# Kernel optimization log

Measured on AMD Instinct MI355X. Metric: run time of the kernel, lower is better.

Reference implementation:

```python
import jax, jax.numpy as jnp
import numpy as np

B, S, SK = 4, 1024, 1024
Q_IN, KV_IN = 1024, 1024
G, DQ, DV = 16, 64, 64
OUT = Q_IN
EPS = 1e-5


def setup_inputs() -> dict:
    key = jax.random.key(0)
    ks = jax.random.split(key, 12)
    s_q = 1.0 / np.sqrt(Q_IN)
    s_kv = 1.0 / np.sqrt(KV_IN)
    s_p = 1.0 / np.sqrt(G * DV)
    return {
        "Q": jax.random.normal(ks[0], (B, S, Q_IN), jnp.float32),
        "KV": jax.random.normal(ks[1], (B, SK, KV_IN), jnp.float32),
        "Wq": jax.random.normal(ks[2], (G * DQ, Q_IN), jnp.float32) * s_q,
        "bq": jax.random.normal(ks[3], (G * DQ,), jnp.float32) * s_q,
        "Wk": jax.random.normal(ks[4], (G * DQ, KV_IN), jnp.float32) * s_kv,
        "bk": jax.random.normal(ks[5], (G * DQ,), jnp.float32) * s_kv,
        "Wv": jax.random.normal(ks[6], (G * DV, KV_IN), jnp.float32) * s_kv,
        "bv": jax.random.normal(ks[7], (G * DV,), jnp.float32) * s_kv,
        "Wp": jax.random.normal(ks[8], (OUT, G * DV), jnp.float32) * s_p,
        "bp": jax.random.normal(ks[9], (OUT,), jnp.float32) * s_p,
        "gamma": jnp.ones((OUT,), jnp.float32),
        "beta": jnp.zeros((OUT,), jnp.float32),
    }


def reference(Q, KV, Wq, bq, Wk, bk, Wv, bv, Wp, bp, gamma, beta):
    b, s, _ = Q.shape
    sk = KV.shape[1]
    inv_sqrt_dim = DQ ** (-0.5)

    # projections
    q = Q @ Wq.T + bq            # [b, s, G*DQ]
    k = KV @ Wk.T + bk           # [b, sk, G*DQ]
    v = KV @ Wv.T + bv           # [b, sk, G*DV]

    # q/k: group is the SLOW axis; v: group is the FAST axis (faithful to source)
    q = q.reshape(b, s, G, DQ)               # [b, s, g, d]
    k = k.reshape(b, sk, G, DQ)              # [b, sk, g, d]
    v = v.reshape(b, sk, DV, G)              # [b, sk, d, g]

    logits = jnp.einsum('bsgd,btgd->bgst', q, k) * inv_sqrt_dim  # [b, g, s, sk]
    scores = jax.nn.softmax(logits, axis=-1)
    attn = jnp.einsum('bgst,btdg->bgsd', scores, v)              # [b, g, s, dv]

    # flatten as (dv, g): feature index = d*G + g  (faithful to source permute)
    attn = attn.transpose(0, 2, 3, 1).reshape(b, s, DV * G)
    out = attn @ Wp.T + bp + Q

    # LayerNorm
    mu = out.mean(axis=-1, keepdims=True)
    var = out.var(axis=-1, keepdims=True)
    out = (out - mu) * jax.lax.rsqrt(var + EPS) * gamma + beta

    return out, scores.reshape(b * G, s, sk)
```

## Files before the change

kernel.cpp:

```cpp
#include <hip/hip_runtime.h>

typedef __attribute__((ext_vector_type(8))) short short8;
typedef __attribute__((ext_vector_type(4))) short s16x4;
typedef __attribute__((ext_vector_type(4))) float f32x4;

static __device__ __forceinline__ short f2bf(float x) {
  union { float f; unsigned u; } v; v.f = x;
  unsigned r = (v.u + 0x7fffu + ((v.u >> 16) & 1u)) >> 16;
  return (short)r;
}
static __device__ __forceinline__ float bf2f(short x) {
  union { unsigned u; float f; } v; v.u = ((unsigned)(unsigned short)x) << 16;
  return v.f;
}

static __device__ __forceinline__ void gld16(const short* g, short* l) {
  __builtin_amdgcn_global_load_lds(
      (const __attribute__((address_space(1))) unsigned*)g,
      (__attribute__((address_space(3))) unsigned*)l, 16, 0, 0);
}

static __device__ __forceinline__ void conv8(const float* __restrict__ src,
                                             short* __restrict__ dst, int i,
                                             float scale) {
  const f32x4* s = (const f32x4*)(src + (long)i * 8);
  f32x4 a = s[0], b = s[1];
  short8 o;
  o[0] = f2bf(a[0] * scale); o[1] = f2bf(a[1] * scale);
  o[2] = f2bf(a[2] * scale); o[3] = f2bf(a[3] * scale);
  o[4] = f2bf(b[0] * scale); o[5] = f2bf(b[1] * scale);
  o[6] = f2bf(b[2] * scale); o[7] = f2bf(b[3] * scale);
  *(short8*)(dst + (long)i * 8) = o;
}

__global__ __launch_bounds__(256) void prep(
    const float* __restrict__ Q, const float* __restrict__ KV,
    const float* __restrict__ Wq, const float* __restrict__ Wk,
    const float* __restrict__ Wv, const float* __restrict__ Wp,
    const float* __restrict__ bq,
    short* __restrict__ Qb, short* __restrict__ KVb,
    short* __restrict__ Wqb, short* __restrict__ Wkb,
    short* __restrict__ Wvb, short* __restrict__ Wpb,
    float* __restrict__ bqs) {
  const int blk = blockIdx.x, tid = threadIdx.x;
  if (blk < 2048) {
    conv8(Q, Qb, blk * 256 + tid, 1.f);
  } else if (blk < 4096) {
    conv8(KV, KVb, (blk - 2048) * 256 + tid, 1.f);
  } else if (blk < 4608) {
    conv8(Wq, Wqb, (blk - 4096) * 256 + tid, 0.125f);
  } else if (blk < 5120) {
    conv8(Wk, Wkb, (blk - 4608) * 256 + tid, 1.f);
  } else if (blk < 5632) {
    conv8(Wv, Wvb, (blk - 5120) * 256 + tid, 1.f);
  } else if (blk < 6656) {
    __shared__ float row[1024];
    const long o = blk - 5632;
    *(f32x4*)&row[tid * 4] = *(const f32x4*)(Wp + o * 1024 + tid * 4);
    __syncthreads();
    const int f0 = tid * 4;
    s16x4 t;
#pragma unroll
    for (int j = 0; j < 4; ++j) {
      int f = f0 + j;
      t[j] = f2bf(row[((f & 63) << 4) + (f >> 6)]);
    }
    *(s16x4*)(Wpb + o * 1024 + f0) = t;
  } else {
    int i = (blk - 6656) * 256 + tid;
    bqs[i] = bq[i] * 0.125f;
  }
}

template <typename OutT>
static __device__ __forceinline__ void gemm_core(
    const short* __restrict__ A, const short* __restrict__ B,
    OutT* __restrict__ C, const float* __restrict__ bias,
    const float* __restrict__ resid, int bm, int bn, int omode,
    short (*As)[128 * 64], short (*Bs)[128 * 64]) {
  const int tid = threadIdx.x, lane = tid & 63, wave = tid >> 6;
  const int fr = lane & 15, khi = lane >> 4;
  const int wr = wave >> 1, wc = wave & 1;

  f32x4 acc[4][4];
#pragma unroll
  for (int m = 0; m < 4; ++m)
#pragma unroll
    for (int n = 0; n < 4; ++n) acc[m][n] = (f32x4){0.f, 0.f, 0.f, 0.f};

  auto stage = [&](int buf, int k0) {
#pragma unroll
    for (int it = 0; it < 4; ++it) {
      int l = it * 256 + tid;
      int r = l >> 3, c = (l & 7) ^ (r & 7);
      gld16(A + (long)(bm + r) * 1024 + k0 + c * 8, &As[buf][l * 8]);
      gld16(B + (long)(bn + r) * 1024 + k0 + c * 8, &Bs[buf][l * 8]);
    }
  };

  stage(0, 0);
  __syncthreads();
  int cur = 0;
  for (int k0 = 0; k0 < 1024; k0 += 64) {
    if (k0 < 960) stage(cur ^ 1, k0 + 64);
#pragma unroll
    for (int ks = 0; ks < 64; ks += 32) {
      const int cc = (ks >> 3) + khi;
      short8 af[4], bf[4];
#pragma unroll
      for (int m = 0; m < 4; ++m) {
        const int ar = wr * 64 + m * 16 + fr;
        af[m] = *(const short8*)&As[cur][ar * 64 + ((cc ^ (ar & 7)) * 8)];
      }
#pragma unroll
      for (int n = 0; n < 4; ++n) {
        const int br = wc * 64 + n * 16 + fr;
        bf[n] = *(const short8*)&Bs[cur][br * 64 + ((cc ^ (br & 7)) * 8)];
      }
#pragma unroll
      for (int m = 0; m < 4; ++m)
#pragma unroll
        for (int n = 0; n < 4; ++n)
          acc[m][n] = __builtin_amdgcn_mfma_f32_16x16x32_bf16(af[m], bf[n],
                                                              acc[m][n], 0, 0, 0);
    }
    __syncthreads();
    cur ^= 1;
  }

  const int col0 = lane & 15, row0 = (lane >> 4) * 4;
#pragma unroll
  for (int m = 0; m < 4; ++m) {
#pragma unroll
    for (int n = 0; n < 4; ++n) {
      const int gcol = bn + wc * 64 + n * 16 + col0;
      const float bi = bias[gcol];
#pragma unroll
      for (int i = 0; i < 4; ++i) {
        const int grow = bm + wr * 64 + m * 16 + row0 + i;
        float v = acc[m][n][i] + bi;
        if (resid) v += resid[(long)grow * 1024 + gcol];
        long addr;
        if (omode == 0)
          addr = (long)grow * 1024 + gcol;
        else
          addr = ((long)(grow >> 10) << 20) + ((long)gcol << 10) + (grow & 1023);
        if constexpr (sizeof(OutT) == 2)
          C[addr] = (OutT)f2bf(v);
        else
          C[addr] = v;
      }
    }
  }
}

__global__ __launch_bounds__(256, 2) void proj_all(
    const short* __restrict__ Qb, const short* __restrict__ KVb,
    const short* __restrict__ Wqb, const short* __restrict__ Wkb,
    const short* __restrict__ Wvb,
    const float* __restrict__ bqs, const float* __restrict__ bk,
    const float* __restrict__ bv,
    short* __restrict__ qb, short* __restrict__ kb, short* __restrict__ vt) {
  __shared__ short As[2][128 * 64];
  __shared__ short Bs[2][128 * 64];
  int bid = blockIdx.x;
  int swz = (bid & 7) * 96 + (bid >> 3);
  const int seg = swz >> 8, local = swz & 255;
  const int bm = (local >> 3) * 128, bn = (local & 7) * 128;
  if (seg == 0)
    gemm_core<short>(Qb, Wqb, qb, bqs, nullptr, bm, bn, 0, As, Bs);
  else if (seg == 1)
    gemm_core<short>(KVb, Wkb, kb, bk, nullptr, bm, bn, 0, As, Bs);
  else
    gemm_core<short>(KVb, Wvb, vt, bv, nullptr, bm, bn, 1, As, Bs);
}

__global__ __launch_bounds__(256, 2) void out_gemm(
    const short* __restrict__ at, const short* __restrict__ Wpb,
    const float* __restrict__ bp, const float* __restrict__ Q,
    float* __restrict__ pre) {
  __shared__ short As[2][128 * 64];
  __shared__ short Bs[2][128 * 64];
  int bid = blockIdx.x;
  int swz = (bid & 7) * 32 + (bid >> 3);
  const int bm = (swz >> 3) * 128, bn = (swz & 7) * 128;
  gemm_core<float>(at, Wpb, pre, bp, Q, bm, bn, 0, As, Bs);
}

__global__ __launch_bounds__(512, 6) void fused_attn(
    const short* __restrict__ qb,
    const short* __restrict__ kb,
    const short* __restrict__ vt,
    float* __restrict__ scores,
    short* __restrict__ at) {
  constexpr int LP = 72;
  __shared__ short Ks[2][64 * 64];
  __shared__ short Vs[2][64 * 64];
  __shared__ short Ps[128 * LP];

  int bid = blockIdx.x;
  bid = (bid & 7) * 64 + (bid >> 3);
  const int z = bid >> 3, b = z >> 4, g = z & 15;
  const int q0 = (bid & 7) * 128;

  const int tid = threadIdx.x, lane = tid & 63, w = tid >> 6;
  const int fr = lane & 15, khi = lane >> 4;
  const long bqk = (long)b << 20;
  const int qr = q0 + w * 16;

  const short* qrow = qb + bqk + (long)(qr + fr) * 1024 + g * 64 + khi * 8;
  const short8 aq0 = *(const short8*)qrow;
  const short8 aq1 = *(const short8*)(qrow + 32);
  const short* kgp = kb + bqk + g * 64;
  const short* vgp = vt + bqk;

  const int srr = tid >> 3, ssc = ((tid & 7) ^ (srr & 7)) * 8;

  float s4[4] = {0.f, 0.f, 0.f, 0.f};
  gld16(kgp + (long)srr * 1024 + ssc, &Ks[0][tid * 8]);
  __syncthreads();
  int cur = 0;
  for (int t0 = 0; t0 < 1024; t0 += 64) {
    if (t0 < 960)
      gld16(kgp + (long)(t0 + 64 + srr) * 1024 + ssc, &Ks[cur ^ 1][tid * 8]);
    f32x4 sacc[4];
#pragma unroll
    for (int nf = 0; nf < 4; ++nf) sacc[nf] = (f32x4){0.f, 0.f, 0.f, 0.f};
#pragma unroll
    for (int nf = 0; nf < 4; ++nf) {
      const int r2 = nf * 16 + fr;
      short8 b0 = *(const short8*)&Ks[cur][r2 * 64 + (khi ^ (r2 & 7)) * 8];
      short8 b1 = *(const short8*)&Ks[cur][r2 * 64 + ((khi + 4) ^ (r2 & 7)) * 8];
      sacc[nf] = __builtin_amdgcn_mfma_f32_16x16x32_bf16(aq0, b0, sacc[nf], 0, 0, 0);
      sacc[nf] = __builtin_amdgcn_mfma_f32_16x16x32_bf16(aq1, b1, sacc[nf], 0, 0, 0);
    }
#pragma unroll
    for (int nf = 0; nf < 4; ++nf)
#pragma unroll
      for (int i = 0; i < 4; ++i) s4[i] += __expf(sacc[nf][i]);
    __syncthreads();
    cur ^= 1;
  }
#pragma unroll
  for (int i = 0; i < 4; ++i) {
    s4[i] += __shfl_xor(s4[i], 1);
    s4[i] += __shfl_xor(s4[i], 2);
    s4[i] += __shfl_xor(s4[i], 4);
    s4[i] += __shfl_xor(s4[i], 8);
  }
  float inv4[4];
#pragma unroll
  for (int i = 0; i < 4; ++i) inv4[i] = 1.f / s4[i];

  f32x4 pacc[4];
#pragma unroll
  for (int nv = 0; nv < 4; ++nv) pacc[nv] = (f32x4){0.f, 0.f, 0.f, 0.f};

  gld16(kgp + (long)srr * 1024 + ssc, &Ks[0][tid * 8]);
  gld16(vgp + ((long)(srr * 16 + g) << 10) + ssc, &Vs[0][tid * 8]);
  __syncthreads();
  cur = 0;
  for (int t0 = 0; t0 < 1024; t0 += 64) {
    if (t0 < 960) {
      gld16(kgp + (long)(t0 + 64 + srr) * 1024 + ssc, &Ks[cur ^ 1][tid * 8]);
      gld16(vgp + ((long)(srr * 16 + g) << 10) + t0 + 64 + ssc, &Vs[cur ^ 1][tid * 8]);
    }
    f32x4 sacc[4];
#pragma unroll
    for (int nf = 0; nf < 4; ++nf) sacc[nf] = (f32x4){0.f, 0.f, 0.f, 0.f};
#pragma unroll
    for (int nf = 0; nf < 4; ++nf) {
      const int r2 = nf * 16 + fr;
      short8 b0 = *(const short8*)&Ks[cur][r2 * 64 + (khi ^ (r2 & 7)) * 8];
      short8 b1 = *(const short8*)&Ks[cur][r2 * 64 + ((khi + 4) ^ (r2 & 7)) * 8];
      sacc[nf] = __builtin_amdgcn_mfma_f32_16x16x32_bf16(aq0, b0, sacc[nf], 0, 0, 0);
      sacc[nf] = __builtin_amdgcn_mfma_f32_16x16x32_bf16(aq1, b1, sacc[nf], 0, 0, 0);
    }
#pragma unroll
    for (int nf = 0; nf < 4; ++nf)
#pragma unroll
      for (int i = 0; i < 4; ++i)
        Ps[(w * 16 + khi * 4 + i) * LP + nf * 16 + fr] =
            f2bf(__expf(sacc[nf][i]) * inv4[i]);

#pragma unroll
    for (int ks = 0; ks < 64; ks += 32) {
      const int cc = (ks >> 3) + khi;
      short8 ap = *(const short8*)&Ps[(w * 16 + fr) * LP + ks + khi * 8];
#pragma unroll
      for (int nv = 0; nv < 4; ++nv) {
        const int dr = nv * 16 + fr;
        short8 bvv = *(const short8*)&Vs[cur][dr * 64 + (cc ^ (dr & 7)) * 8];
        pacc[nv] = __builtin_amdgcn_mfma_f32_16x16x32_bf16(ap, bvv, pacc[nv], 0, 0, 0);
      }
    }

#pragma unroll
    for (int ri = 0; ri < 4; ++ri) {
      const int row = ri * 4 + khi;
      s16x4 pv4 = *(const s16x4*)&Ps[(w * 16 + row) * LP + fr * 4];
      f32x4 o;
      o[0] = bf2f(pv4[0]); o[1] = bf2f(pv4[1]);
      o[2] = bf2f(pv4[2]); o[3] = bf2f(pv4[3]);
      *(f32x4*)&scores[((long)z << 20) + ((long)(qr + row) << 10) + t0 + fr * 4] = o;
    }
    __syncthreads();
    cur ^= 1;
  }

#pragma unroll
  for (int nv = 0; nv < 4; ++nv)
#pragma unroll
    for (int i = 0; i < 4; ++i)
      at[bqk + ((long)(qr + khi * 4 + i) << 10) + g * 64 + nv * 16 + fr] =
          f2bf(pacc[nv][i]);
}

__global__ __launch_bounds__(256) void layernorm_rows(const float* __restrict__ X,
                                                      const float* __restrict__ gamma,
                                                      const float* __restrict__ beta,
                                                      float* __restrict__ O) {
  const int row = blockIdx.x * 4 + (threadIdx.x >> 6);
  const int lane = threadIdx.x & 63;
  const float* x = X + (long)row * 1024 + lane * 4;
  f32x4 v[4];
  float s = 0.f, sq = 0.f;
#pragma unroll
  for (int j = 0; j < 4; ++j) {
    v[j] = *(const f32x4*)(x + j * 256);
#pragma unroll
    for (int e = 0; e < 4; ++e) {
      s += v[j][e];
      sq += v[j][e] * v[j][e];
    }
  }
#pragma unroll
  for (int off = 32; off; off >>= 1) {
    s += __shfl_xor(s, off);
    sq += __shfl_xor(sq, off);
  }
  const float mu = s * (1.f / 1024.f);
  const float var = sq * (1.f / 1024.f) - mu * mu;
  const float rstd = rsqrtf(var + 1e-5f);
  float* o = O + (long)row * 1024 + lane * 4;
#pragma unroll
  for (int j = 0; j < 4; ++j) {
    f32x4 g = *(const f32x4*)(gamma + lane * 4 + j * 256);
    f32x4 be = *(const f32x4*)(beta + lane * 4 + j * 256);
    f32x4 r;
#pragma unroll
    for (int e = 0; e < 4; ++e) r[e] = (v[j][e] - mu) * rstd * g[e] + be[e];
    *(f32x4*)(o + j * 256) = r;
  }
}

extern "C" void kernel_launch(void* const* d_in, const int* in_sizes, int n_in,
                              void* d_out, int out_size, void* d_ws, size_t ws_size,
                              hipStream_t stream) {
  const float* Q = (const float*)d_in[0];
  const float* KV = (const float*)d_in[1];
  const float* Wq = (const float*)d_in[2];
  const float* bq = (const float*)d_in[3];
  const float* Wk = (const float*)d_in[4];
  const float* bk = (const float*)d_in[5];
  const float* Wv = (const float*)d_in[6];
  const float* bv = (const float*)d_in[7];
  const float* Wp = (const float*)d_in[8];
  const float* bp = (const float*)d_in[9];
  const float* gamma = (const float*)d_in[10];
  const float* beta = (const float*)d_in[11];

  float* out = (float*)d_out;
  float* scores = out + (long)4 * 1024 * 1024;

  char* ws = (char*)d_ws;
  short* Wqb = (short*)(ws);
  short* Wkb = (short*)(ws + (2L << 20));
  short* Wvb = (short*)(ws + (4L << 20));
  short* Wpb = (short*)(ws + (6L << 20));
  short* qb  = (short*)(ws + (8L << 20));
  short* kb  = (short*)(ws + (16L << 20));
  short* vt  = (short*)(ws + (24L << 20));
  short* at  = (short*)(ws + (32L << 20));
  float* pre = (float*)(ws + (40L << 20));
  short* Qb  = (short*)(ws + (40L << 20));
  short* KVb = (short*)(ws + (48L << 20));
  float* bqs = (float*)(ws + (56L << 20));
  (void)ws_size; (void)in_sizes; (void)n_in; (void)out_size;

  prep<<<6660, 256, 0, stream>>>(Q, KV, Wq, Wk, Wv, Wp, bq,
                                 Qb, KVb, Wqb, Wkb, Wvb, Wpb, bqs);

  proj_all<<<768, 256, 0, stream>>>(Qb, KVb, Wqb, Wkb, Wvb, bqs, bk, bv,
                                    qb, kb, vt);

  fused_attn<<<512, 512, 0, stream>>>(qb, kb, vt, scores, at);

  out_gemm<<<256, 256, 0, stream>>>(at, Wpb, bp, Q, pre);

  layernorm_rows<<<1024, 256, 0, stream>>>(pre, gamma, beta, out);
}
```

Before: 179.2 us.

## Give each attention wave 32 query rows and halve the block size

The fused attention kernel now runs 256 threads (4 waves) per block, and each wave handles two 16-row query sub-tiles instead of one. Every K and V fragment read from LDS is therefore reused for two MFMAs, and each thread stages two K/V chunks per tile. Scores writes become nontemporal stores so the large probability output does not pollute cache. The cost is more registers per wave and fewer waves per block, which may reduce latency hiding.

```diff
diff --git a/kernel.cpp b/kernel.cpp
--- a/kernel.cpp
+++ b/kernel.cpp
@@ -187,7 +187,7 @@
   gemm_core<float>(at, Wpb, pre, bp, Q, bm, bn, 0, As, Bs);
 }
 
-__global__ __launch_bounds__(512, 6) void fused_attn(
+__global__ __launch_bounds__(256, 3) void fused_attn(
     const short* __restrict__ qb,
     const short* __restrict__ kb,
     const short* __restrict__ vt,
@@ -206,114 +206,143 @@
   const int tid = threadIdx.x, lane = tid & 63, w = tid >> 6;
   const int fr = lane & 15, khi = lane >> 4;
   const long bqk = (long)b << 20;
-  const int qr = q0 + w * 16;
-
-  const short* qrow = qb + bqk + (long)(qr + fr) * 1024 + g * 64 + khi * 8;
-  const short8 aq0 = *(const short8*)qrow;
-  const short8 aq1 = *(const short8*)(qrow + 32);
+  const int qr = q0 + w * 32;
+
+  short8 aq[4];
+#pragma unroll
+  for (int sub = 0; sub < 2; ++sub) {
+    const short* qrow = qb + bqk + (long)(qr + sub * 16 + fr) * 1024 + g * 64 + khi * 8;
+    aq[sub * 2] = *(const short8*)qrow;
+    aq[sub * 2 + 1] = *(const short8*)(qrow + 32);
+  }
   const short* kgp = kb + bqk + g * 64;
   const short* vgp = vt + bqk;
 
-  const int srr = tid >> 3, ssc = ((tid & 7) ^ (srr & 7)) * 8;
-
-  float s4[4] = {0.f, 0.f, 0.f, 0.f};
-  gld16(kgp + (long)srr * 1024 + ssc, &Ks[0][tid * 8]);
+  auto stageK = [&](int buf, int t0) {
+#pragma unroll
+    for (int it = 0; it < 2; ++it) {
+      int l = it * 256 + tid;
+      int r = l >> 3, c = (l & 7) ^ (r & 7);
+      gld16(kgp + (long)(t0 + r) * 1024 + c * 8, &Ks[buf][l * 8]);
+    }
+  };
+  auto stageV = [&](int buf, int t0) {
+#pragma unroll
+    for (int it = 0; it < 2; ++it) {
+      int l = it * 256 + tid;
+      int r = l >> 3, c = (l & 7) ^ (r & 7);
+      gld16(vgp + ((long)(r * 16 + g) << 10) + t0 + c * 8, &Vs[buf][l * 8]);
+    }
+  };
+
+  float s4[2][4] = {{0.f, 0.f, 0.f, 0.f}, {0.f, 0.f, 0.f, 0.f}};
+  stageK(0, 0);
   __syncthreads();
   int cur = 0;
   for (int t0 = 0; t0 < 1024; t0 += 64) {
-    if (t0 < 960)
-      gld16(kgp + (long)(t0 + 64 + srr) * 1024 + ssc, &Ks[cur ^ 1][tid * 8]);
-    f32x4 sacc[4];
-#pragma unroll
-    for (int nf = 0; nf < 4; ++nf) sacc[nf] = (f32x4){0.f, 0.f, 0.f, 0.f};
+    if (t0 < 960) stageK(cur ^ 1, t0 + 64);
 #pragma unroll
     for (int nf = 0; nf < 4; ++nf) {
       const int r2 = nf * 16 + fr;
       short8 b0 = *(const short8*)&Ks[cur][r2 * 64 + (khi ^ (r2 & 7)) * 8];
       short8 b1 = *(const short8*)&Ks[cur][r2 * 64 + ((khi + 4) ^ (r2 & 7)) * 8];
-      sacc[nf] = __builtin_amdgcn_mfma_f32_16x16x32_bf16(aq0, b0, sacc[nf], 0, 0, 0);
-      sacc[nf] = __builtin_amdgcn_mfma_f32_16x16x32_bf16(aq1, b1, sacc[nf], 0, 0, 0);
-    }
-#pragma unroll
-    for (int nf = 0; nf < 4; ++nf)
-#pragma unroll
-      for (int i = 0; i < 4; ++i) s4[i] += __expf(sacc[nf][i]);
+#pragma unroll
+      for (int sub = 0; sub < 2; ++sub) {
+        f32x4 sacc = (f32x4){0.f, 0.f, 0.f, 0.f};
+        sacc = __builtin_amdgcn_mfma_f32_16x16x32_bf16(aq[sub * 2], b0, sacc, 0, 0, 0);
+        sacc = __builtin_amdgcn_mfma_f32_16x16x32_bf16(aq[sub * 2 + 1], b1, sacc, 0, 0, 0);
+#pragma unroll
+        for (int i = 0; i < 4; ++i) s4[sub][i] += __expf(sacc[i]);
+      }
+    }
     __syncthreads();
     cur ^= 1;
   }
-#pragma unroll
-  for (int i = 0; i < 4; ++i) {
-    s4[i] += __shfl_xor(s4[i], 1);
-    s4[i] += __shfl_xor(s4[i], 2);
-    s4[i] += __shfl_xor(s4[i], 4);
-    s4[i] += __shfl_xor(s4[i], 8);
-  }
-  float inv4[4];
-#pragma unroll
-  for (int i = 0; i < 4; ++i) inv4[i] = 1.f / s4[i];
-
-  f32x4 pacc[4];
-#pragma unroll
-  for (int nv = 0; nv < 4; ++nv) pacc[nv] = (f32x4){0.f, 0.f, 0.f, 0.f};
-
-  gld16(kgp + (long)srr * 1024 + ssc, &Ks[0][tid * 8]);
-  gld16(vgp + ((long)(srr * 16 + g) << 10) + ssc, &Vs[0][tid * 8]);
+  float inv4[2][4];
+#pragma unroll
+  for (int sub = 0; sub < 2; ++sub)
+#pragma unroll
+    for (int i = 0; i < 4; ++i) {
+      float s = s4[sub][i];
+      s += __shfl_xor(s, 1);
+      s += __shfl_xor(s, 2);
+      s += __shfl_xor(s, 4);
+      s += __shfl_xor(s, 8);
+      inv4[sub][i] = 1.f / s;
+    }
+
+  f32x4 pacc[2][4];
+#pragma unroll
+  for (int sub = 0; sub < 2; ++sub)
+#pragma unroll
+    for (int nv = 0; nv < 4; ++nv) pacc[sub][nv] = (f32x4){0.f, 0.f, 0.f, 0.f};
+
+  stageK(0, 0);
+  stageV(0, 0);
   __syncthreads();
   cur = 0;
   for (int t0 = 0; t0 < 1024; t0 += 64) {
     if (t0 < 960) {
-      gld16(kgp + (long)(t0 + 64 + srr) * 1024 + ssc, &Ks[cur ^ 1][tid * 8]);
-      gld16(vgp + ((long)(srr * 16 + g) << 10) + t0 + 64 + ssc, &Vs[cur ^ 1][tid * 8]);
-    }
-    f32x4 sacc[4];
-#pragma unroll
-    for (int nf = 0; nf < 4; ++nf) sacc[nf] = (f32x4){0.f, 0.f, 0.f, 0.f};
+      stageK(cur ^ 1, t0 + 64);
+      stageV(cur ^ 1, t0 + 64);
+    }
 #pragma unroll
     for (int nf = 0; nf < 4; ++nf) {
       const int r2 = nf * 16 + fr;
       short8 b0 = *(const short8*)&Ks[cur][r2 * 64 + (khi ^ (r2 & 7)) * 8];
       short8 b1 = *(const short8*)&Ks[cur][r2 * 64 + ((khi + 4) ^ (r2 & 7)) * 8];
-      sacc[nf] = __builtin_amdgcn_mfma_f32_16x16x32_bf16(aq0, b0, sacc[nf], 0, 0, 0);
-      sacc[nf] = __builtin_amdgcn_mfma_f32_16x16x32_bf16(aq1, b1, sacc[nf], 0, 0, 0);
-    }
-#pragma unroll
-    for (int nf = 0; nf < 4; ++nf)
-#pragma unroll
-      for (int i = 0; i < 4; ++i)
-        Ps[(w * 16 + khi * 4 + i) * LP + nf * 16 + fr] =
-            f2bf(__expf(sacc[nf][i]) * inv4[i]);
+#pragma unroll
+      for (int sub = 0; sub < 2; ++sub) {
+        f32x4 sacc = (f32x4){0.f, 0.f, 0.f, 0.f};
+        sacc = __builtin_amdgcn_mfma_f32_16x16x32_bf16(aq[sub * 2], b0, sacc, 0, 0, 0);
+        sacc = __builtin_amdgcn_mfma_f32_16x16x32_bf16(aq[sub * 2 + 1], b1, sacc, 0, 0, 0);
+#pragma unroll
+        for (int i = 0; i < 4; ++i)
+          Ps[(w * 32 + sub * 16 + khi * 4 + i) * LP + nf * 16 + fr] =
+              f2bf(__expf(sacc[i]) * inv4[sub][i]);
+      }
+    }
 
 #pragma unroll
     for (int ks = 0; ks < 64; ks += 32) {
       const int cc = (ks >> 3) + khi;
-      short8 ap = *(const short8*)&Ps[(w * 16 + fr) * LP + ks + khi * 8];
+      short8 ap[2];
+#pragma unroll
+      for (int sub = 0; sub < 2; ++sub)
+        ap[sub] = *(const short8*)&Ps[(w * 32 + sub * 16 + fr) * LP + ks + khi * 8];
 #pragma unroll
       for (int nv = 0; nv < 4; ++nv) {
         const int dr = nv * 16 + fr;
         short8 bvv = *(const short8*)&Vs[cur][dr * 64 + (cc ^ (dr & 7)) * 8];
-        pacc[nv] = __builtin_amdgcn_mfma_f32_16x16x32_bf16(ap, bvv, pacc[nv], 0, 0, 0);
-      }
-    }
-
-#pragma unroll
-    for (int ri = 0; ri < 4; ++ri) {
+#pragma unroll
+        for (int sub = 0; sub < 2; ++sub)
+          pacc[sub][nv] =
+              __builtin_amdgcn_mfma_f32_16x16x32_bf16(ap[sub], bvv, pacc[sub][nv], 0, 0, 0);
+      }
+    }
+
+#pragma unroll
+    for (int ri = 0; ri < 8; ++ri) {
       const int row = ri * 4 + khi;
-      s16x4 pv4 = *(const s16x4*)&Ps[(w * 16 + row) * LP + fr * 4];
+      s16x4 pv4 = *(const s16x4*)&Ps[(w * 32 + row) * LP + fr * 4];
       f32x4 o;
       o[0] = bf2f(pv4[0]); o[1] = bf2f(pv4[1]);
       o[2] = bf2f(pv4[2]); o[3] = bf2f(pv4[3]);
-      *(f32x4*)&scores[((long)z << 20) + ((long)(qr + row) << 10) + t0 + fr * 4] = o;
+      __builtin_nontemporal_store(
+          o, (f32x4*)&scores[((long)z << 20) + ((long)(qr + row) << 10) + t0 + fr * 4]);
     }
     __syncthreads();
     cur ^= 1;
   }
 
 #pragma unroll
-  for (int nv = 0; nv < 4; ++nv)
-#pragma unroll
-    for (int i = 0; i < 4; ++i)
-      at[bqk + ((long)(qr + khi * 4 + i) << 10) + g * 64 + nv * 16 + fr] =
-          f2bf(pacc[nv][i]);
+  for (int sub = 0; sub < 2; ++sub)
+#pragma unroll
+    for (int nv = 0; nv < 4; ++nv)
+#pragma unroll
+      for (int i = 0; i < 4; ++i)
+        at[bqk + ((long)(qr + sub * 16 + khi * 4 + i) << 10) + g * 64 + nv * 16 + fr] =
+            f2bf(pacc[sub][nv][i]);
 }
 
 __global__ __launch_bounds__(256) void layernorm_rows(const float* __restrict__ X,
@@ -394,7 +423,7 @@
   proj_all<<<768, 256, 0, stream>>>(Qb, KVb, Wqb, Wkb, Wvb, bqs, bk, bv,
                                     qb, kb, vt);
 
-  fused_attn<<<512, 512, 0, stream>>>(qb, kb, vt, scores, at);
+  fused_attn<<<512, 256, 0, stream>>>(qb, kb, vt, scores, at);
 
   out_gemm<<<256, 256, 0, stream>>>(at, Wpb, bp, Q, pre);
 
```

After: 178.3 us. No clear change (-0.5%).
